# Optimization experiments

Measured on AMD Instinct MI355X. Metric: run time of the kernel, lower is better.

## Reference

```python
import jax, jax.numpy as jnp
import numpy as np
from jax.ops import segment_sum, segment_max

N_NODES, N_EDGES, N_GRAPHS = 50000, 800000, 128
IN_C, HID, HEADS, CLIN = 64, 64, 4, 32


def gat_layer(x, W, a_s, a_d, b, src, dst, n):
    # GAT-style attention conv with concatenated heads (PyG GATConv math).
    H, C = a_s.shape
    h = (x @ W).reshape(-1, H, C)                      # [N,H,C]
    es = jnp.einsum('nhc,hc->nh', h, a_s)
    ed = jnp.einsum('nhc,hc->nh', h, a_d)
    e = jax.nn.leaky_relu(es[src] + ed[dst], 0.2)      # [E,H]
    m = segment_max(e, dst, num_segments=n)            # stable softmax over incoming edges
    e = jnp.exp(e - m[dst])
    denom = segment_sum(e, dst, num_segments=n)
    alpha = e / jnp.where(denom[dst] > 0, denom[dst], 1.0)
    out = segment_sum(h[src] * alpha[:, :, None], dst, num_segments=n)  # [N,H,C]
    return out.reshape(-1, H * C) + b


def label_prop(x, src, dst, n, num_layers=2, alpha=0.5):
    # PyG LabelPropagation: sym-normalized diffusion, residual mix, clamp to [0,1].
    deg = segment_sum(jnp.ones((src.shape[0],), x.dtype), dst, num_segments=n)
    dis = jnp.where(deg > 0, 1.0 / jnp.sqrt(jnp.maximum(deg, 1.0)), 0.0)
    norm = (dis[src] * dis[dst])[:, None]
    res = (1.0 - alpha) * x
    out = x
    for _ in range(num_layers):
        out = alpha * segment_sum(out[src] * norm, dst, num_segments=n) + res
        out = jnp.clip(out, 0.0, 1.0)
    return out


def mean_pool(x, batch, n_graphs):
    cnt = segment_sum(jnp.ones((x.shape[0],), x.dtype), batch, num_segments=n_graphs)
    s = segment_sum(x, batch, num_segments=n_graphs)
    return s / jnp.maximum(cnt, 1.0)[:, None]


def setup_inputs() -> dict:
    key = jax.random.key(0)
    ks = iter(jax.random.split(key, 32))
    def p(shape, fan_in):
        return jax.random.normal(next(ks), shape, jnp.float32) / np.sqrt(fan_in)
    d = {}
    d['x'] = jax.random.normal(next(ks), (N_NODES, IN_C), jnp.float32)
    d['edge_index'] = jax.random.randint(next(ks), (2, N_EDGES), 0, N_NODES)
    d['batch'] = jnp.sort(jax.random.randint(next(ks), (N_NODES,), 0, N_GRAPHS))
    d['clinical_data'] = jax.random.normal(next(ks), (N_GRAPHS, CLIN), jnp.float32)
    HC = HEADS * HID
    d['W1'] = p((IN_C, HC), IN_C); d['a1s'] = p((HEADS, HID), HID); d['a1d'] = p((HEADS, HID), HID); d['b1'] = jnp.zeros((HC,), jnp.float32)
    d['W2'] = p((HC, HC), HC); d['a2s'] = p((HEADS, HID), HID); d['a2d'] = p((HEADS, HID), HID); d['b2'] = jnp.zeros((HC,), jnp.float32)
    jk = IN_C + 2 * HC  # 576
    d['pp_w1'] = p((jk, 256), jk); d['pp_b1'] = jnp.zeros((256,), jnp.float32)
    d['pp_w2'] = p((256, 128), 256); d['pp_b2'] = jnp.zeros((128,), jnp.float32)
    d['cl_w1'] = p((CLIN, 64), CLIN); d['cl_b1'] = jnp.zeros((64,), jnp.float32)
    d['cl_w2'] = p((64, 32), 64); d['cl_b2'] = jnp.zeros((32,), jnp.float32)
    d['h_w1'] = p((160, 64), 160); d['h_b1'] = jnp.zeros((64,), jnp.float32)
    d['h_w2'] = p((64, 32), 64); d['h_b2'] = jnp.zeros((32,), jnp.float32)
    d['h_w3'] = p((32, 2), 32); d['h_b3'] = jnp.zeros((2,), jnp.float32)
    return d


def reference(x, edge_index, batch, clinical_data,
              W1, a1s, a1d, b1, W2, a2s, a2d, b2,
              pp_w1, pp_b1, pp_w2, pp_b2,
              cl_w1, cl_b1, cl_w2, cl_b2,
              h_w1, h_b1, h_w2, h_b2, h_w3, h_b3):
    src, dst = edge_index[0], edge_index[1]
    n = x.shape[0]
    h0 = x
    h1 = jax.nn.relu(gat_layer(h0, W1, a1s, a1d, b1, src, dst, n))
    h1 = label_prop(h1, src, dst, n)
    h2 = jax.nn.relu(gat_layer(h1, W2, a2s, a2d, b2, src, dst, n))
    h2 = label_prop(h2, src, dst, n)
    combined = jnp.concatenate([h0, h1, h2], axis=-1)           # [N, 576]
    g = mean_pool(combined, batch, N_GRAPHS)                    # [G, 576]
    v_graph = jax.nn.relu(g @ pp_w1 + pp_b1) @ pp_w2 + pp_b2    # [G, 128] (dropout = eval/no-op)
    v_clin = jax.nn.relu(clinical_data @ cl_w1 + cl_b1) @ cl_w2 + cl_b2  # [G, 32]
    z = jnp.concatenate([v_graph, v_clin], axis=-1)             # [G, 160]
    z = jax.nn.relu(z @ h_w1 + h_b1)
    z = jax.nn.relu(z @ h_w2 + h_b2)
    return z @ h_w3 + h_b3                                      # [G, 2]
```

## Files before the change

kernel.cpp:

```cpp
#include <hip/hip_runtime.h>

#define N_NODES 50000
#define N_EDGES 800000
#define N_GRAPHS 128
#define JK 576
#define CAP 192
#define NSB ((N_NODES + 255) / 256)

typedef __attribute__((ext_vector_type(8))) short bf16x8;
typedef __attribute__((ext_vector_type(4))) float f32x4;

__device__ __forceinline__ unsigned f2_to_bf2(float a, float b) {
    unsigned ua = __float_as_uint(a), ub = __float_as_uint(b);
    ua = (ua + 0x7fffu + ((ua >> 16) & 1u)) >> 16;
    ub = (ub + 0x7fffu + ((ub >> 16) & 1u)) >> 16;
    return ua | (ub << 16);
}
__device__ __forceinline__ uint2 f4_to_bf4(float4 v) {
    return make_uint2(f2_to_bf2(v.x, v.y), f2_to_bf2(v.z, v.w));
}
__device__ __forceinline__ float4 bf4_to_f4(uint2 u) {
    float4 r;
    r.x = __uint_as_float(u.x << 16);
    r.y = __uint_as_float(u.x & 0xffff0000u);
    r.z = __uint_as_float(u.y << 16);
    r.w = __uint_as_float(u.y & 0xffff0000u);
    return r;
}

template<int BN, int KK>
__global__ __launch_bounds__(256)
void mfma_gemm(const unsigned short* __restrict__ Abf, int lda,
               const unsigned short* __restrict__ BT,
               unsigned* __restrict__ Cbf, int ldc,
               int M, const float* __restrict__ bias, int relu,
               int a_off, int b_off, int c_off) {
    __shared__ unsigned short As[64][32];
    __shared__ unsigned short Bs[BN][32];
    const int t = threadIdx.x;
    const int wav = t >> 6, lane = t & 63;
    const int quad = lane >> 4, l15 = lane & 15;
    const int m0 = blockIdx.x * 64;
    const int head = blockIdx.y;
    Abf += (size_t)head * a_off;
    BT  += (size_t)head * b_off;
    const float* bptr = bias ? bias + (size_t)head * c_off : nullptr;
    unsigned* cbf = Cbf + (((size_t)head * c_off) >> 1);

    f32x4 acc[BN / 16];
#pragma unroll
    for (int i = 0; i < BN / 16; i++) acc[i] = (f32x4){0.f, 0.f, 0.f, 0.f};

    const int arow = t >> 2, aseg = t & 3;
    for (int k0 = 0; k0 < KK; k0 += 32) {
        uint4 av = make_uint4(0, 0, 0, 0);
        int gm = m0 + arow;
        if (gm < M) av = *(const uint4*)&Abf[(size_t)gm * lda + k0 + aseg * 8];
        uint4 bv[BN == 256 ? 4 : 1];
        if (BN == 256) {
            const unsigned short* srcb = &BT[(size_t)t * KK + k0];
#pragma unroll
            for (int j = 0; j < 4; j++) bv[j] = *(const uint4*)&srcb[j * 8];
        } else {
            bv[0] = *(const uint4*)&BT[(size_t)arow * KK + k0 + aseg * 8];
        }
        __syncthreads();
        *(uint4*)&As[arow][aseg * 8] = av;
        if (BN == 256) {
#pragma unroll
            for (int j = 0; j < 4; j++) *(uint4*)&Bs[t][j * 8] = bv[j];
        } else {
            *(uint4*)&Bs[arow][aseg * 8] = bv[0];
        }
        __syncthreads();
        bf16x8 afrag = *(const bf16x8*)&As[wav * 16 + l15][quad * 8];
#pragma unroll
        for (int nt = 0; nt < BN / 16; nt++) {
            bf16x8 bfrag = *(const bf16x8*)&Bs[nt * 16 + l15][quad * 8];
            acc[nt] = __builtin_amdgcn_mfma_f32_16x16x32_bf16(afrag, bfrag, acc[nt], 0, 0, 0);
        }
    }
    int rbase = m0 + wav * 16 + quad * 4;
#pragma unroll
    for (int nt = 0; nt < BN / 16; nt++) {
        int col = nt * 16 + l15;
        float bb = bptr ? bptr[col] : 0.f;
#pragma unroll
        for (int r = 0; r < 4; r++) {
            int row = rbase + r;
            float v = acc[nt][r] + bb;
            if (relu) v = fmaxf(v, 0.f);
            float vp = __shfl_xor(v, 1);
            if (row < M && !(l15 & 1))
                cbf[((size_t)row * ldc + col) >> 1] = f2_to_bf2(v, vp);
        }
    }
}

__global__ void conv_wT(const float* __restrict__ W, unsigned short* __restrict__ WT,
                        int IN, int OUT) {
    int i = blockIdx.x * blockDim.x + threadIdx.x;
    if (i >= IN * OUT) return;
    int n = i / IN, c = i - n * IN;
    unsigned u = __float_as_uint(W[(size_t)c * OUT + n]);
    u = (u + 0x7fffu + ((u >> 16) & 1u)) >> 16;
    WT[i] = (unsigned short)u;
}

__global__ void deg_kernel(const int* __restrict__ dst, int* __restrict__ deg) {
    int t = blockIdx.x * blockDim.x + threadIdx.x;
    if (t < N_EDGES) atomicAdd(&deg[dst[t]], 1);
}
__global__ void dis_kernel(const int* __restrict__ deg, float* __restrict__ dis) {
    int i = blockIdx.x * blockDim.x + threadIdx.x;
    if (i >= N_NODES) return;
    int d = deg[i];
    dis[i] = d > 0 ? rsqrtf((float)d) : 0.f;
}
__global__ __launch_bounds__(256) void scan_bsum(const int* __restrict__ deg,
                                                 int* __restrict__ bsum) {
    __shared__ int sd[256];
    int n = blockIdx.x * 256 + threadIdx.x;
    sd[threadIdx.x] = (n < N_NODES) ? deg[n] : 0;
    __syncthreads();
    for (int o = 128; o > 0; o >>= 1) {
        if (threadIdx.x < o) sd[threadIdx.x] += sd[threadIdx.x + o];
        __syncthreads();
    }
    if (threadIdx.x == 0) bsum[blockIdx.x] = sd[0];
}
__global__ __launch_bounds__(256) void scan_bpre(const int* __restrict__ bsum,
                                                 int* __restrict__ bpre,
                                                 int* __restrict__ off_last) {
    __shared__ int sd[256];
    int t = threadIdx.x;
    int v = (t < NSB) ? bsum[t] : 0;
    sd[t] = v;
    __syncthreads();
    for (int o = 1; o < 256; o <<= 1) {
        int u = (t >= o) ? sd[t - o] : 0;
        __syncthreads();
        sd[t] += u;
        __syncthreads();
    }
    if (t < NSB) bpre[t] = sd[t] - v;
    if (t == 255) *off_last = sd[255];
}
__global__ __launch_bounds__(256) void scan_off(const int* __restrict__ deg,
                                                const int* __restrict__ bpre,
                                                int* __restrict__ off) {
    __shared__ int sd[256];
    int n = blockIdx.x * 256 + threadIdx.x;
    int t = threadIdx.x;
    int v = (n < N_NODES) ? deg[n] : 0;
    sd[t] = v;
    __syncthreads();
    for (int o = 1; o < 256; o <<= 1) {
        int u = (t >= o) ? sd[t - o] : 0;
        __syncthreads();
        sd[t] += u;
        __syncthreads();
    }
    if (n < N_NODES) off[n] = bpre[blockIdx.x] + sd[t] - v;
}
__global__ void csr_fill(const int* __restrict__ src, const int* __restrict__ dst,
                         const int* __restrict__ off, int* __restrict__ cursor,
                         int* __restrict__ csr_src) {
    int e = blockIdx.x * blockDim.x + threadIdx.x;
    if (e >= N_EDGES) return;
    int s = src[e], d = dst[e];
    int pos = off[d] + atomicAdd(&cursor[d], 1);
    csr_src[pos] = s;
}

__global__ void prep_w(const float* __restrict__ W, const float* __restrict__ as_,
                       const float* __restrict__ ad_, float* __restrict__ wes,
                       float* __restrict__ wed, int K) {
    int t = blockIdx.x * blockDim.x + threadIdx.x;
    if (t >= K * 4) return;
    int c = t >> 2, h = t & 3;
    float se = 0.f, sd = 0.f;
    for (int j = 0; j < 64; j++) {
        float w = W[(size_t)c * 256 + h * 64 + j];
        se += w * as_[h * 64 + j];
        sd += w * ad_[h * 64 + j];
    }
    wes[c * 4 + h] = se;
    wed[c * 4 + h] = sd;
}

__global__ void esed_x(const float* __restrict__ X, const float* __restrict__ wes,
                       const float* __restrict__ wed, float* __restrict__ es,
                       float* __restrict__ ed) {
    int gid = blockIdx.x * blockDim.x + threadIdx.x;
    int n = gid >> 6, lane = threadIdx.x & 63;
    if (n >= N_NODES) return;
    float xv = X[(size_t)n * 64 + lane];
    float4 a = *(const float4*)&wes[lane * 4];
    float4 b = *(const float4*)&wed[lane * 4];
    float4 ps = make_float4(xv * a.x, xv * a.y, xv * a.z, xv * a.w);
    float4 pd = make_float4(xv * b.x, xv * b.y, xv * b.z, xv * b.w);
#pragma unroll
    for (int o = 1; o < 64; o <<= 1) {
        ps.x += __shfl_xor(ps.x, o); ps.y += __shfl_xor(ps.y, o);
        ps.z += __shfl_xor(ps.z, o); ps.w += __shfl_xor(ps.w, o);
        pd.x += __shfl_xor(pd.x, o); pd.y += __shfl_xor(pd.y, o);
        pd.z += __shfl_xor(pd.z, o); pd.w += __shfl_xor(pd.w, o);
    }
    if (lane == 0) {
        *(float4*)&es[n * 4] = ps;
        *(float4*)&ed[n * 4] = pd;
    }
}

__global__ void esed_h(const unsigned* __restrict__ Hbf, const float* __restrict__ wes,
                       const float* __restrict__ wed, float* __restrict__ es,
                       float* __restrict__ ed) {
    int gid = blockIdx.x * blockDim.x + threadIdx.x;
    int n = gid >> 6, lane = threadIdx.x & 63;
    if (n >= N_NODES) return;
    float4 xv = bf4_to_f4(*(const uint2*)&Hbf[(size_t)n * 128 + lane * 2]);
    float xs[4] = {xv.x, xv.y, xv.z, xv.w};
    float4 ps = make_float4(0.f, 0.f, 0.f, 0.f);
    float4 pd = make_float4(0.f, 0.f, 0.f, 0.f);
#pragma unroll
    for (int r = 0; r < 4; r++) {
        int c = lane * 4 + r;
        float4 a = *(const float4*)&wes[c * 4];
        float4 b = *(const float4*)&wed[c * 4];
        ps.x += xs[r] * a.x; ps.y += xs[r] * a.y; ps.z += xs[r] * a.z; ps.w += xs[r] * a.w;
        pd.x += xs[r] * b.x; pd.y += xs[r] * b.y; pd.z += xs[r] * b.z; pd.w += xs[r] * b.w;
    }
#pragma unroll
    for (int o = 1; o < 64; o <<= 1) {
        ps.x += __shfl_xor(ps.x, o); ps.y += __shfl_xor(ps.y, o);
        ps.z += __shfl_xor(ps.z, o); ps.w += __shfl_xor(ps.w, o);
        pd.x += __shfl_xor(pd.x, o); pd.y += __shfl_xor(pd.y, o);
        pd.z += __shfl_xor(pd.z, o); pd.w += __shfl_xor(pd.w, o);
    }
    if (lane == 0) {
        *(float4*)&es[n * 4] = ps;
        *(float4*)&ed[n * 4] = pd;
    }
}

__global__ __launch_bounds__(256)
void gat1_fused(const int* __restrict__ off, const int* __restrict__ csr_src,
                const float* __restrict__ es, const float* __restrict__ ed,
                const float* __restrict__ x, unsigned* __restrict__ aggx_bf,
                float* __restrict__ alpha_fb) {
    __shared__ float elds[4][CAP * 4];
    __shared__ int   sidx[4][CAP];
    int wav = threadIdx.x >> 6, lane = threadIdx.x & 63;
    int n = blockIdx.x * 4 + wav;
    bool active = n < N_NODES;
    int p0 = 0, p1 = 0;
    float4 ed4 = make_float4(0.f, 0.f, 0.f, 0.f);
    if (active) { p0 = off[n]; p1 = off[n + 1]; ed4 = *(const float4*)&ed[n * 4]; }
    float4 sum = make_float4(0.f, 0.f, 0.f, 0.f);
    for (int p = p0 + lane; p < p1; p += 64) {
        int s = csr_src[p];
        float4 e4 = *(const float4*)&es[s * 4];
        e4.x += ed4.x; e4.y += ed4.y; e4.z += ed4.z; e4.w += ed4.w;
        e4.x = e4.x > 0.f ? e4.x : 0.2f * e4.x;
        e4.y = e4.y > 0.f ? e4.y : 0.2f * e4.y;
        e4.z = e4.z > 0.f ? e4.z : 0.2f * e4.z;
        e4.w = e4.w > 0.f ? e4.w : 0.2f * e4.w;
        e4.x = __expf(e4.x); e4.y = __expf(e4.y); e4.z = __expf(e4.z); e4.w = __expf(e4.w);
        int q = p - p0;
        if (q < CAP) { *(float4*)&elds[wav][q * 4] = e4; sidx[wav][q] = s; }
        else         *(float4*)&alpha_fb[(size_t)p * 4] = e4;
        sum.x += e4.x; sum.y += e4.y; sum.z += e4.z; sum.w += e4.w;
    }
#pragma unroll
    for (int o = 1; o < 64; o <<= 1) {
        sum.x += __shfl_xor(sum.x, o); sum.y += __shfl_xor(sum.y, o);
        sum.z += __shfl_xor(sum.z, o); sum.w += __shfl_xor(sum.w, o);
    }
    float4 rs;
    rs.x = sum.x > 0.f ? 1.f / sum.x : 0.f;
    rs.y = sum.y > 0.f ? 1.f / sum.y : 0.f;
    rs.z = sum.z > 0.f ? 1.f / sum.z : 0.f;
    rs.w = sum.w > 0.f ? 1.f / sum.w : 0.f;
    if (!active) return;
    int eg = lane >> 4, l15 = lane & 15;
    int deg = p1 - p0;
    float4 a0 = make_float4(0.f, 0.f, 0.f, 0.f);
    float4 a1 = a0, a2 = a0, a3 = a0;
    int q = eg;
    float4 eA = make_float4(0.f, 0.f, 0.f, 0.f);
    float4 xA = eA;
    if (q < deg) {
        int s;
        if (q < CAP) { s = sidx[wav][q]; eA = *(const float4*)&elds[wav][q * 4]; }
        else { s = csr_src[p0 + q]; eA = *(const float4*)&alpha_fb[(size_t)(p0 + q) * 4]; }
        xA = *(const float4*)&x[(size_t)s * 64 + l15 * 4];
    }
    while (q < deg) {
        int qn = q + 4;
        float4 eB = make_float4(0.f, 0.f, 0.f, 0.f);
        float4 xB = eB;
        if (qn < deg) {
            int s;
            if (qn < CAP) { s = sidx[wav][qn]; eB = *(const float4*)&elds[wav][qn * 4]; }
            else { s = csr_src[p0 + qn]; eB = *(const float4*)&alpha_fb[(size_t)(p0 + qn) * 4]; }
            xB = *(const float4*)&x[(size_t)s * 64 + l15 * 4];
        }
        a0.x += eA.x * xA.x; a0.y += eA.x * xA.y; a0.z += eA.x * xA.z; a0.w += eA.x * xA.w;
        a1.x += eA.y * xA.x; a1.y += eA.y * xA.y; a1.z += eA.y * xA.z; a1.w += eA.y * xA.w;
        a2.x += eA.z * xA.x; a2.y += eA.z * xA.y; a2.z += eA.z * xA.z; a2.w += eA.z * xA.w;
        a3.x += eA.w * xA.x; a3.y += eA.w * xA.y; a3.z += eA.w * xA.z; a3.w += eA.w * xA.w;
        eA = eB; xA = xB; q = qn;
    }
#pragma unroll
    for (int o = 16; o < 64; o <<= 1) {
        a0.x += __shfl_xor(a0.x, o); a0.y += __shfl_xor(a0.y, o);
        a0.z += __shfl_xor(a0.z, o); a0.w += __shfl_xor(a0.w, o);
        a1.x += __shfl_xor(a1.x, o); a1.y += __shfl_xor(a1.y, o);
        a1.z += __shfl_xor(a1.z, o); a1.w += __shfl_xor(a1.w, o);
        a2.x += __shfl_xor(a2.x, o); a2.y += __shfl_xor(a2.y, o);
        a2.z += __shfl_xor(a2.z, o); a2.w += __shfl_xor(a2.w, o);
        a3.x += __shfl_xor(a3.x, o); a3.y += __shfl_xor(a3.y, o);
        a3.z += __shfl_xor(a3.z, o); a3.w += __shfl_xor(a3.w, o);
    }
    if (eg == 0) {
        a0.x *= rs.x; a0.y *= rs.x; a0.z *= rs.x; a0.w *= rs.x;
        a1.x *= rs.y; a1.y *= rs.y; a1.z *= rs.y; a1.w *= rs.y;
        a2.x *= rs.z; a2.y *= rs.z; a2.z *= rs.z; a2.w *= rs.z;
        a3.x *= rs.w; a3.y *= rs.w; a3.z *= rs.w; a3.w *= rs.w;
        size_t b = (size_t)n * 128 + l15 * 2;
        *(uint2*)&aggx_bf[b +  0] = f4_to_bf4(a0);
        *(uint2*)&aggx_bf[b + 32] = f4_to_bf4(a1);
        *(uint2*)&aggx_bf[b + 64] = f4_to_bf4(a2);
        *(uint2*)&aggx_bf[b + 96] = f4_to_bf4(a3);
    }
}

__global__ __launch_bounds__(256)
void gat2_fused(const int* __restrict__ off, const int* __restrict__ csr_src,
                const float* __restrict__ es, const float* __restrict__ ed,
                const unsigned* __restrict__ H2bf, const float* __restrict__ bias,
                unsigned* __restrict__ outbf, float* __restrict__ alpha_fb) {
    __shared__ float elds[4][CAP * 4];
    __shared__ int   sidx[4][CAP];
    int wav = threadIdx.x >> 6, lane = threadIdx.x & 63;
    int n = blockIdx.x * 4 + wav;
    bool active = n < N_NODES;
    int p0 = 0, p1 = 0;
    float4 ed4 = make_float4(0.f, 0.f, 0.f, 0.f);
    if (active) { p0 = off[n]; p1 = off[n + 1]; ed4 = *(const float4*)&ed[n * 4]; }
    float4 sum = make_float4(0.f, 0.f, 0.f, 0.f);
    for (int p = p0 + lane; p < p1; p += 64) {
        int s = csr_src[p];
        float4 e4 = *(const float4*)&es[s * 4];
        e4.x += ed4.x; e4.y += ed4.y; e4.z += ed4.z; e4.w += ed4.w;
        e4.x = e4.x > 0.f ? e4.x : 0.2f * e4.x;
        e4.y = e4.y > 0.f ? e4.y : 0.2f * e4.y;
        e4.z = e4.z > 0.f ? e4.z : 0.2f * e4.z;
        e4.w = e4.w > 0.f ? e4.w : 0.2f * e4.w;
        e4.x = __expf(e4.x); e4.y = __expf(e4.y); e4.z = __expf(e4.z); e4.w = __expf(e4.w);
        int q = p - p0;
        if (q < CAP) { *(float4*)&elds[wav][q * 4] = e4; sidx[wav][q] = s; }
        else         *(float4*)&alpha_fb[(size_t)p * 4] = e4;
        sum.x += e4.x; sum.y += e4.y; sum.z += e4.z; sum.w += e4.w;
    }
#pragma unroll
    for (int o = 1; o < 64; o <<= 1) {
        sum.x += __shfl_xor(sum.x, o); sum.y += __shfl_xor(sum.y, o);
        sum.z += __shfl_xor(sum.z, o); sum.w += __shfl_xor(sum.w, o);
    }
    if (!active) return;
    int half = lane >> 5, l = lane & 31;
    int hh = l >> 3;
    float sh = (hh == 0) ? sum.x : (hh == 1) ? sum.y : (hh == 2) ? sum.z : sum.w;
    float rsh = sh > 0.f ? 1.f / sh : 0.f;
    int deg = p1 - p0;
    float acc[8];
#pragma unroll
    for (int j = 0; j < 8; j++) acc[j] = 0.f;
    int q = half;
    float aA = 0.f;
    uint4 rA = make_uint4(0, 0, 0, 0);
    if (q < deg) {
        int s;
        if (q < CAP) { s = sidx[wav][q]; aA = elds[wav][q * 4 + hh]; }
        else { s = csr_src[p0 + q]; aA = alpha_fb[(size_t)(p0 + q) * 4 + hh]; }
        rA = *(const uint4*)&H2bf[(size_t)s * 128 + l * 4];
    }
    while (q < deg) {
        int qn = q + 2;
        float aB = 0.f;
        uint4 rB = make_uint4(0, 0, 0, 0);
        if (qn < deg) {
            int s;
            if (qn < CAP) { s = sidx[wav][qn]; aB = elds[wav][qn * 4 + hh]; }
            else { s = csr_src[p0 + qn]; aB = alpha_fb[(size_t)(p0 + qn) * 4 + hh]; }
            rB = *(const uint4*)&H2bf[(size_t)s * 128 + l * 4];
        }
        float4 f0 = bf4_to_f4(make_uint2(rA.x, rA.y));
        float4 f1 = bf4_to_f4(make_uint2(rA.z, rA.w));
        acc[0] += aA * f0.x; acc[1] += aA * f0.y; acc[2] += aA * f0.z; acc[3] += aA * f0.w;
        acc[4] += aA * f1.x; acc[5] += aA * f1.y; acc[6] += aA * f1.z; acc[7] += aA * f1.w;
        aA = aB; rA = rB; q = qn;
    }
#pragma unroll
    for (int j = 0; j < 8; j++) acc[j] += __shfl_xor(acc[j], 32);
    if (half == 0) {
        float4 b0 = *(const float4*)&bias[l * 8];
        float4 b1 = *(const float4*)&bias[l * 8 + 4];
        float4 o0, o1;
        o0.x = fmaxf(acc[0] * rsh + b0.x, 0.f);
        o0.y = fmaxf(acc[1] * rsh + b0.y, 0.f);
        o0.z = fmaxf(acc[2] * rsh + b0.z, 0.f);
        o0.w = fmaxf(acc[3] * rsh + b0.w, 0.f);
        o1.x = fmaxf(acc[4] * rsh + b1.x, 0.f);
        o1.y = fmaxf(acc[5] * rsh + b1.y, 0.f);
        o1.z = fmaxf(acc[6] * rsh + b1.z, 0.f);
        o1.w = fmaxf(acc[7] * rsh + b1.w, 0.f);
        uint2 w0 = f4_to_bf4(o0), w1 = f4_to_bf4(o1);
        uint4 w = make_uint4(w0.x, w0.y, w1.x, w1.y);
        *(uint4*)&outbf[(size_t)n * 128 + l * 4] = w;
    }
}

__global__ __launch_bounds__(256)
void lp_csr(const int* __restrict__ off, const int* __restrict__ csr_src,
            const float* __restrict__ dis, const unsigned* __restrict__ in_bf,
            const unsigned* __restrict__ res_bf, unsigned* __restrict__ out_bf) {
    __shared__ int   widx[4][CAP];
    __shared__ float wwt[4][CAP];
    int wav = threadIdx.x >> 6, lane = threadIdx.x & 63;
    int n = blockIdx.x * 4 + wav;
    if (n >= N_NODES) return;
    int p0 = off[n], p1 = off[n + 1];
    int deg = p1 - p0;
    float disd = dis[n];
    for (int q = lane; q < deg && q < CAP; q += 64) {
        int s = csr_src[p0 + q];
        widx[wav][q] = s;
        wwt[wav][q] = dis[s] * disd;
    }
    int half = lane >> 5, l = lane & 31;
    float acc[8];
#pragma unroll
    for (int j = 0; j < 8; j++) acc[j] = 0.f;
    int q = half;
    float nA = 0.f;
    uint4 rA = make_uint4(0, 0, 0, 0);
    if (q < deg) {
        int s;
        if (q < CAP) { s = widx[wav][q]; nA = wwt[wav][q]; }
        else { s = csr_src[p0 + q]; nA = dis[s] * disd; }
        rA = *(const uint4*)&in_bf[(size_t)s * 128 + l * 4];
    }
    while (q < deg) {
        int qn = q + 2;
        float nB = 0.f;
        uint4 rB = make_uint4(0, 0, 0, 0);
        if (qn < deg) {
            int s;
            if (qn < CAP) { s = widx[wav][qn]; nB = wwt[wav][qn]; }
            else { s = csr_src[p0 + qn]; nB = dis[s] * disd; }
            rB = *(const uint4*)&in_bf[(size_t)s * 128 + l * 4];
        }
        float4 f0 = bf4_to_f4(make_uint2(rA.x, rA.y));
        float4 f1 = bf4_to_f4(make_uint2(rA.z, rA.w));
        acc[0] += nA * f0.x; acc[1] += nA * f0.y; acc[2] += nA * f0.z; acc[3] += nA * f0.w;
        acc[4] += nA * f1.x; acc[5] += nA * f1.y; acc[6] += nA * f1.z; acc[7] += nA * f1.w;
        nA = nB; rA = rB; q = qn;
    }
#pragma unroll
    for (int j = 0; j < 8; j++) acc[j] += __shfl_xor(acc[j], 32);
    if (half == 0) {
        uint4 rr = *(const uint4*)&res_bf[(size_t)n * 128 + l * 4];
        float4 r0 = bf4_to_f4(make_uint2(rr.x, rr.y));
        float4 r1 = bf4_to_f4(make_uint2(rr.z, rr.w));
        float4 o0, o1;
        o0.x = fminf(fmaxf(0.5f * acc[0] + 0.5f * r0.x, 0.f), 1.f);
        o0.y = fminf(fmaxf(0.5f * acc[1] + 0.5f * r0.y, 0.f), 1.f);
        o0.z = fminf(fmaxf(0.5f * acc[2] + 0.5f * r0.z, 0.f), 1.f);
        o0.w = fminf(fmaxf(0.5f * acc[3] + 0.5f * r0.w, 0.f), 1.f);
        o1.x = fminf(fmaxf(0.5f * acc[4] + 0.5f * r1.x, 0.f), 1.f);
        o1.y = fminf(fmaxf(0.5f * acc[5] + 0.5f * r1.y, 0.f), 1.f);
        o1.z = fminf(fmaxf(0.5f * acc[6] + 0.5f * r1.z, 0.f), 1.f);
        o1.w = fminf(fmaxf(0.5f * acc[7] + 0.5f * r1.w, 0.f), 1.f);
        uint2 w0 = f4_to_bf4(o0), w1 = f4_to_bf4(o1);
        uint4 w = make_uint4(w0.x, w0.y, w1.x, w1.y);
        *(uint4*)&out_bf[(size_t)n * 128 + l * 4] = w;
    }
}

__global__ void bounds_kernel(const int* __restrict__ batch, int* __restrict__ gstart) {
    int n = blockIdx.x * blockDim.x + threadIdx.x;
    if (n >= N_NODES) return;
    int b = batch[n];
    int prev = (n == 0) ? -1 : batch[n - 1];
    for (int g = prev + 1; g <= b; g++) gstart[g] = n;
    if (n == N_NODES - 1)
        for (int g = b + 1; g <= N_GRAPHS; g++) gstart[g] = N_NODES;
}
__global__ void pool_partial(const float* __restrict__ buf, const int* __restrict__ gstart,
                             float* __restrict__ psum, int C, int colOff) {
    int g = blockIdx.x, q = blockIdx.y;
    int n0 = gstart[g], n1 = gstart[g + 1];
    int len = n1 - n0;
    int ns = n0 + (len * q) / 4, ne = n0 + (len * (q + 1)) / 4;
    int cp = threadIdx.x % C;
    int np = threadIdx.x / C;
    int NP = 256 / C;
    float s = 0.f;
    for (int n = ns + np; n < ne; n += NP) s += buf[(size_t)n * C + cp];
    atomicAdd(&psum[g * JK + colOff + cp], s);
}
__global__ void pool_bf(const unsigned* __restrict__ buf, const int* __restrict__ gstart,
                        float* __restrict__ psum, int colOff) {
    int g = blockIdx.x, q = blockIdx.y;
    int n0 = gstart[g], n1 = gstart[g + 1];
    int len = n1 - n0;
    int ns = n0 + (len * q) / 4, ne = n0 + (len * (q + 1)) / 4;
    int cp = threadIdx.x & 127;
    int np = threadIdx.x >> 7;
    float s0 = 0.f, s1 = 0.f;
    for (int n = ns + np; n < ne; n += 2) {
        unsigned u = buf[(size_t)n * 128 + cp];
        s0 += __uint_as_float(u << 16);
        s1 += __uint_as_float(u & 0xffff0000u);
    }
    atomicAdd(&psum[g * JK + colOff + cp * 2 + 0], s0);
    atomicAdd(&psum[g * JK + colOff + cp * 2 + 1], s1);
}
__global__ void gmean_kernel(const float* __restrict__ psum, const int* __restrict__ gstart,
                             float* __restrict__ g) {
    int i = blockIdx.x * blockDim.x + threadIdx.x;
    if (i >= N_GRAPHS * JK) return;
    int gi = i / JK;
    int len = gstart[gi + 1] - gstart[gi];
    g[i] = psum[i] / (float)(len > 1 ? len : 1);
}

__global__ __launch_bounds__(64)
void head_d1(const float* __restrict__ gbuf, const float* __restrict__ W,
             const float* __restrict__ bias, float* __restrict__ out) {
    __shared__ float zin[JK];
    int g = blockIdx.y, mc = blockIdx.x, lane = threadIdx.x;
    for (int k = lane; k < JK; k += 64) zin[k] = gbuf[g * JK + k];
    __syncthreads();
    int m = mc * 64 + lane;
    float acc = bias[m];
#pragma unroll 8
    for (int k = 0; k < JK; k++) acc += zin[k] * W[k * 256 + m];
    out[g * 256 + m] = fmaxf(acc, 0.f);
}

__global__ __launch_bounds__(256)
void head_rest(const float* __restrict__ t1, const float* __restrict__ clin,
               const float* __restrict__ pp_w2, const float* __restrict__ pp_b2,
               const float* __restrict__ cl_w1, const float* __restrict__ cl_b1,
               const float* __restrict__ cl_w2, const float* __restrict__ cl_b2,
               const float* __restrict__ h_w1, const float* __restrict__ h_b1,
               const float* __restrict__ h_w2, const float* __restrict__ h_b2,
               const float* __restrict__ h_w3, const float* __restrict__ h_b3,
               float* __restrict__ out) {
    __shared__ float z1[256];
    __shared__ float zcl[32];
    __shared__ float zc[64];
    __shared__ float z[160];
    __shared__ float z3[64];
    __shared__ float z4[32];
    __shared__ float part[128];
    int g = blockIdx.x, t = threadIdx.x;
    z1[t] = t1[g * 256 + t];
    if (t < 32) zcl[t] = clin[g * 32 + t];
    __syncthreads();
    int m = t & 127, half = t >> 7;
    {
        float acc = 0.f;
        int k0 = half * 128;
#pragma unroll 8
        for (int k = k0; k < k0 + 128; k++) acc += z1[k] * pp_w2[k * 128 + m];
        if (half) part[m] = acc;
        __syncthreads();
        if (!half) z[m] = acc + part[m] + pp_b2[m];
    }
    if (t < 64) {
        float acc = cl_b1[t];
#pragma unroll
        for (int k = 0; k < 32; k++) acc += zcl[k] * cl_w1[k * 64 + t];
        zc[t] = fmaxf(acc, 0.f);
    }
    __syncthreads();
    if (t < 32) {
        float acc = cl_b2[t];
#pragma unroll
        for (int k = 0; k < 64; k++) acc += zc[k] * cl_w2[k * 32 + t];
        z[128 + t] = acc;
    }
    __syncthreads();
    if (t < 64) {
        float acc = h_b1[t];
#pragma unroll 8
        for (int k = 0; k < 160; k++) acc += z[k] * h_w1[k * 64 + t];
        z3[t] = fmaxf(acc, 0.f);
    }
    __syncthreads();
    if (t < 32) {
        float acc = h_b2[t];
#pragma unroll
        for (int k = 0; k < 64; k++) acc += z3[k] * h_w2[k * 32 + t];
        z4[t] = fmaxf(acc, 0.f);
    }
    __syncthreads();
    if (t < 2) {
        float acc = h_b3[t];
#pragma unroll
        for (int k = 0; k < 32; k++) acc += z4[k] * h_w3[k * 2 + t];
        out[g * 2 + t] = acc;
    }
}

extern "C" void kernel_launch(void* const* d_in, const int* in_sizes, int n_in,
                              void* d_out, int out_size, void* d_ws, size_t ws_size,
                              hipStream_t stream) {
    const float* x     = (const float*)d_in[0];
    const int*   ei    = (const int*)d_in[1];
    const int*   batch = (const int*)d_in[2];
    const float* clin  = (const float*)d_in[3];
    const float* W1  = (const float*)d_in[4];
    const float* a1s = (const float*)d_in[5];
    const float* a1d = (const float*)d_in[6];
    const float* b1  = (const float*)d_in[7];
    const float* W2  = (const float*)d_in[8];
    const float* a2s = (const float*)d_in[9];
    const float* a2d = (const float*)d_in[10];
    const float* b2  = (const float*)d_in[11];
    const float* pp_w1 = (const float*)d_in[12];
    const float* pp_b1 = (const float*)d_in[13];
    const float* pp_w2 = (const float*)d_in[14];
    const float* pp_b2 = (const float*)d_in[15];
    const float* cl_w1 = (const float*)d_in[16];
    const float* cl_b1 = (const float*)d_in[17];
    const float* cl_w2 = (const float*)d_in[18];
    const float* cl_b2 = (const float*)d_in[19];
    const float* h_w1  = (const float*)d_in[20];
    const float* h_b1  = (const float*)d_in[21];
    const float* h_w2  = (const float*)d_in[22];
    const float* h_b2  = (const float*)d_in[23];
    const float* h_w3  = (const float*)d_in[24];
    const float* h_b3  = (const float*)d_in[25];

    const int* src = ei;
    const int* dst = ei + N_EDGES;

    char* p = (char*)d_ws;
    auto carve = [&](size_t bytes) -> char* {
        char* r = p;
        p += (bytes + 255) & ~(size_t)255;
        return r;
    };
    const size_t NBH = (size_t)N_NODES * 256 * 2;
    unsigned* abf  = (unsigned*)carve(NBH);
    unsigned* bf1  = (unsigned*)carve(NBH);
    unsigned* bf2  = (unsigned*)carve(NBH);
    unsigned* bf3  = (unsigned*)carve(NBH);
    float* alpha_fb  = (float*)carve((size_t)N_EDGES * 4 * 4);
    int*   csr_src   = (int*)carve((size_t)N_EDGES * 4);
    int*   off       = (int*)carve((size_t)(N_NODES + 1) * 4);
    int*   deg       = (int*)carve((size_t)N_NODES * 4);
    int*   cursor    = (int*)carve((size_t)N_NODES * 4);
    int*   bsum      = (int*)carve((size_t)NSB * 4);
    int*   bpre      = (int*)carve((size_t)NSB * 4);
    float* dis       = (float*)carve((size_t)N_NODES * 4);
    float* es        = (float*)carve((size_t)N_NODES * 4 * 4);
    float* ed        = (float*)carve((size_t)N_NODES * 4 * 4);
    float* wes1      = (float*)carve((size_t)64 * 4 * 4);
    float* wed1      = (float*)carve((size_t)64 * 4 * 4);
    float* wes2      = (float*)carve((size_t)256 * 4 * 4);
    float* wed2      = (float*)carve((size_t)256 * 4 * 4);
    unsigned short* W1T = (unsigned short*)carve((size_t)256 * 64 * 2);
    unsigned short* W2T = (unsigned short*)carve((size_t)256 * 256 * 2);
    int*   gstart    = (int*)carve((size_t)(N_GRAPHS + 1) * 4);
    float* psum      = (float*)carve((size_t)N_GRAPHS * JK * 4);
    float* gbuf      = (float*)carve((size_t)N_GRAPHS * JK * 4);
    float* t1        = (float*)carve((size_t)N_GRAPHS * 256 * 4);

    const int TB = 256;
    const int gN     = (N_NODES + TB - 1) / TB;
    const int gE     = (N_EDGES + TB - 1) / TB;
    const int gNwave = (N_NODES * 64 + TB - 1) / TB;
    const int gFuse  = (N_NODES + 3) / 4;
    const int gRow   = (N_NODES + 63) / 64;

    hipMemsetAsync(deg, 0, (size_t)N_NODES * 4, stream);
    hipMemsetAsync(cursor, 0, (size_t)N_NODES * 4, stream);
    hipMemsetAsync(psum, 0, (size_t)N_GRAPHS * JK * 4, stream);
    deg_kernel<<<gE, TB, 0, stream>>>(dst, deg);
    dis_kernel<<<gN, TB, 0, stream>>>(deg, dis);
    scan_bsum<<<NSB, 256, 0, stream>>>(deg, bsum);
    scan_bpre<<<1, 256, 0, stream>>>(bsum, bpre, &off[N_NODES]);
    scan_off<<<NSB, 256, 0, stream>>>(deg, bpre, off);
    csr_fill<<<gE, TB, 0, stream>>>(src, dst, off, cursor, csr_src);
    bounds_kernel<<<gN, TB, 0, stream>>>(batch, gstart);
    prep_w<<<1, 256, 0, stream>>>(W1, a1s, a1d, wes1, wed1, 64);
    prep_w<<<4, 256, 0, stream>>>(W2, a2s, a2d, wes2, wed2, 256);
    conv_wT<<<(256 * 64 + TB - 1) / TB, TB, 0, stream>>>(W1, W1T, 64, 256);
    conv_wT<<<(256 * 256 + TB - 1) / TB, TB, 0, stream>>>(W2, W2T, 256, 256);

    esed_x<<<gNwave, TB, 0, stream>>>(x, wes1, wed1, es, ed);
    gat1_fused<<<gFuse, TB, 0, stream>>>(off, csr_src, es, ed, x, abf, alpha_fb);
    mfma_gemm<64, 64><<<dim3(gRow, 4), 256, 0, stream>>>(
        (const unsigned short*)abf, 256, W1T, bf1, 256, N_NODES, b1, 1,
        64, 64 * 64, 64);

    lp_csr<<<gFuse, TB, 0, stream>>>(off, csr_src, dis, bf1, bf1, bf2);
    lp_csr<<<gFuse, TB, 0, stream>>>(off, csr_src, dis, bf2, bf1, bf3);

    pool_bf<<<dim3(N_GRAPHS, 4), TB, 0, stream>>>(bf3, gstart, psum, 64);

    mfma_gemm<256, 256><<<dim3(gRow, 1), 256, 0, stream>>>(
        (const unsigned short*)bf3, 256, W2T, bf1, 256, N_NODES, nullptr, 0,
        0, 0, 0);
    esed_h<<<gNwave, TB, 0, stream>>>(bf3, wes2, wed2, es, ed);
    gat2_fused<<<gFuse, TB, 0, stream>>>(off, csr_src, es, ed, bf1, b2, bf2, alpha_fb);

    lp_csr<<<gFuse, TB, 0, stream>>>(off, csr_src, dis, bf2, bf2, bf1);
    lp_csr<<<gFuse, TB, 0, stream>>>(off, csr_src, dis, bf1, bf2, abf);

    pool_partial<<<dim3(N_GRAPHS, 4), TB, 0, stream>>>(x, gstart, psum, 64, 0);
    pool_bf<<<dim3(N_GRAPHS, 4), TB, 0, stream>>>(abf, gstart, psum, 320);
    gmean_kernel<<<(N_GRAPHS * JK + TB - 1) / TB, TB, 0, stream>>>(psum, gstart, gbuf);

    head_d1<<<dim3(4, N_GRAPHS), 64, 0, stream>>>(gbuf, pp_w1, pp_b1, t1);
    head_rest<<<N_GRAPHS, 256, 0, stream>>>(t1, clin, pp_w2, pp_b2, cl_w1, cl_b1,
                                            cl_w2, cl_b2, h_w1, h_b1, h_w2, h_b2,
                                            h_w3, h_b3, (float*)d_out);
}
```

Baseline: 798.3 us.

## Merge prep kernels, gather bf16 features in GAT1, deepen gather prefetch

Folds the small setup kernels (dis, graph bounds, attention weight projection, weight transposes) into one launch. The same launch also converts x to bf16 so GAT layer 1 gathers half as many bytes per neighbour. The gather loops in gat1, gat2 and label propagation now keep three edges of loads in flight instead of one, to hide memory latency. The cost is more registers per thread, and rounding x to bf16 before aggregation adds some precision loss.

```diff
diff --git a/kernel.cpp b/kernel.cpp
--- a/kernel.cpp
+++ b/kernel.cpp
@@ -97,25 +97,78 @@
     }
 }
 
-__global__ void conv_wT(const float* __restrict__ W, unsigned short* __restrict__ WT,
-                        int IN, int OUT) {
-    int i = blockIdx.x * blockDim.x + threadIdx.x;
-    if (i >= IN * OUT) return;
-    int n = i / IN, c = i - n * IN;
-    unsigned u = __float_as_uint(W[(size_t)c * OUT + n]);
-    u = (u + 0x7fffu + ((u >> 16) & 1u)) >> 16;
-    WT[i] = (unsigned short)u;
-}
-
 __global__ void deg_kernel(const int* __restrict__ dst, int* __restrict__ deg) {
     int t = blockIdx.x * blockDim.x + threadIdx.x;
     if (t < N_EDGES) atomicAdd(&deg[dst[t]], 1);
 }
-__global__ void dis_kernel(const int* __restrict__ deg, float* __restrict__ dis) {
+#define S1 50000
+#define S2 100000
+#define S3 100256
+#define S4 101280
+#define S5 117664
+#define S6 183200
+#define S7 1783200
+__global__ void prep_misc(const int* __restrict__ deg, float* __restrict__ dis,
+                          const int* __restrict__ batch, int* __restrict__ gstart,
+                          const float* __restrict__ W1, const float* __restrict__ a1s,
+                          const float* __restrict__ a1d, float* __restrict__ wes1,
+                          float* __restrict__ wed1,
+                          const float* __restrict__ W2, const float* __restrict__ a2s,
+                          const float* __restrict__ a2d, float* __restrict__ wes2,
+                          float* __restrict__ wed2,
+                          unsigned short* __restrict__ W1T, unsigned short* __restrict__ W2T,
+                          const float* __restrict__ x, unsigned* __restrict__ xbf) {
     int i = blockIdx.x * blockDim.x + threadIdx.x;
-    if (i >= N_NODES) return;
-    int d = deg[i];
-    dis[i] = d > 0 ? rsqrtf((float)d) : 0.f;
+    if (i >= S7) return;
+    if (i >= S6) {
+        int j = i - S6;
+        float2 v = *(const float2*)&x[(size_t)j * 2];
+        xbf[j] = f2_to_bf2(v.x, v.y);
+    } else if (i >= S5) {
+        int t2 = i - S5;
+        int n = t2 >> 8, c = t2 & 255;
+        unsigned u = __float_as_uint(W2[(size_t)c * 256 + n]);
+        u = (u + 0x7fffu + ((u >> 16) & 1u)) >> 16;
+        W2T[t2] = (unsigned short)u;
+    } else if (i >= S4) {
+        int t2 = i - S4;
+        int n = t2 >> 6, c = t2 & 63;
+        unsigned u = __float_as_uint(W1[(size_t)c * 256 + n]);
+        u = (u + 0x7fffu + ((u >> 16) & 1u)) >> 16;
+        W1T[t2] = (unsigned short)u;
+    } else if (i >= S3) {
+        int t2 = i - S3;
+        int c = t2 >> 2, h = t2 & 3;
+        float se = 0.f, sd = 0.f;
+        for (int j = 0; j < 64; j++) {
+            float w = W2[(size_t)c * 256 + h * 64 + j];
+            se += w * a2s[h * 64 + j];
+            sd += w * a2d[h * 64 + j];
+        }
+        wes2[c * 4 + h] = se;
+        wed2[c * 4 + h] = sd;
+    } else if (i >= S2) {
+        int t2 = i - S2;
+        int c = t2 >> 2, h = t2 & 3;
+        float se = 0.f, sd = 0.f;
+        for (int j = 0; j < 64; j++) {
+            float w = W1[(size_t)c * 256 + h * 64 + j];
+            se += w * a1s[h * 64 + j];
+            sd += w * a1d[h * 64 + j];
+        }
+        wes1[c * 4 + h] = se;
+        wed1[c * 4 + h] = sd;
+    } else if (i >= S1) {
+        int n = i - S1;
+        int b = batch[n];
+        int prev = (n == 0) ? -1 : batch[n - 1];
+        for (int g = prev + 1; g <= b; g++) gstart[g] = n;
+        if (n == N_NODES - 1)
+            for (int g = b + 1; g <= N_GRAPHS; g++) gstart[g] = N_NODES;
+    } else {
+        int d = deg[i];
+        dis[i] = d > 0 ? rsqrtf((float)d) : 0.f;
+    }
 }
 __global__ __launch_bounds__(256) void scan_bsum(const int* __restrict__ deg,
                                                  int* __restrict__ bsum) {
@@ -171,22 +224,6 @@
     int s = src[e], d = dst[e];
     int pos = off[d] + atomicAdd(&cursor[d], 1);
     csr_src[pos] = s;
-}
-
-__global__ void prep_w(const float* __restrict__ W, const float* __restrict__ as_,
-                       const float* __restrict__ ad_, float* __restrict__ wes,
-                       float* __restrict__ wed, int K) {
-    int t = blockIdx.x * blockDim.x + threadIdx.x;
-    if (t >= K * 4) return;
-    int c = t >> 2, h = t & 3;
-    float se = 0.f, sd = 0.f;
-    for (int j = 0; j < 64; j++) {
-        float w = W[(size_t)c * 256 + h * 64 + j];
-        se += w * as_[h * 64 + j];
-        sd += w * ad_[h * 64 + j];
-    }
-    wes[c * 4 + h] = se;
-    wed[c * 4 + h] = sd;
 }
 
 __global__ void esed_x(const float* __restrict__ X, const float* __restrict__ wes,
@@ -247,7 +284,7 @@
 __global__ __launch_bounds__(256)
 void gat1_fused(const int* __restrict__ off, const int* __restrict__ csr_src,
                 const float* __restrict__ es, const float* __restrict__ ed,
-                const float* __restrict__ x, unsigned* __restrict__ aggx_bf,
+                const unsigned* __restrict__ xbf, unsigned* __restrict__ aggx_bf,
                 float* __restrict__ alpha_fb) {
     __shared__ float elds[4][CAP * 4];
     __shared__ int   sidx[4][CAP];
@@ -287,30 +324,30 @@
     int deg = p1 - p0;
     float4 a0 = make_float4(0.f, 0.f, 0.f, 0.f);
     float4 a1 = a0, a2 = a0, a3 = a0;
+    auto fetch = [&](int qq, float4& e4, float4& xv) {
+        e4 = make_float4(0.f, 0.f, 0.f, 0.f);
+        xv = e4;
+        if (qq < deg) {
+            int s;
+            if (qq < CAP) { s = sidx[wav][qq]; e4 = *(const float4*)&elds[wav][qq * 4]; }
+            else { s = csr_src[p0 + qq]; e4 = *(const float4*)&alpha_fb[(size_t)(p0 + qq) * 4]; }
+            xv = bf4_to_f4(*(const uint2*)&xbf[(size_t)s * 32 + l15 * 2]);
+        }
+    };
     int q = eg;
-    float4 eA = make_float4(0.f, 0.f, 0.f, 0.f);
-    float4 xA = eA;
-    if (q < deg) {
-        int s;
-        if (q < CAP) { s = sidx[wav][q]; eA = *(const float4*)&elds[wav][q * 4]; }
-        else { s = csr_src[p0 + q]; eA = *(const float4*)&alpha_fb[(size_t)(p0 + q) * 4]; }
-        xA = *(const float4*)&x[(size_t)s * 64 + l15 * 4];
-    }
+    float4 eA, xA, eB, xB, eC, xC;
+    fetch(q, eA, xA);
+    fetch(q + 4, eB, xB);
+    fetch(q + 8, eC, xC);
     while (q < deg) {
-        int qn = q + 4;
-        float4 eB = make_float4(0.f, 0.f, 0.f, 0.f);
-        float4 xB = eB;
-        if (qn < deg) {
-            int s;
-            if (qn < CAP) { s = sidx[wav][qn]; eB = *(const float4*)&elds[wav][qn * 4]; }
-            else { s = csr_src[p0 + qn]; eB = *(const float4*)&alpha_fb[(size_t)(p0 + qn) * 4]; }
-            xB = *(const float4*)&x[(size_t)s * 64 + l15 * 4];
-        }
+        float4 eD, xD;
+        fetch(q + 12, eD, xD);
         a0.x += eA.x * xA.x; a0.y += eA.x * xA.y; a0.z += eA.x * xA.z; a0.w += eA.x * xA.w;
         a1.x += eA.y * xA.x; a1.y += eA.y * xA.y; a1.z += eA.y * xA.z; a1.w += eA.y * xA.w;
         a2.x += eA.z * xA.x; a2.y += eA.z * xA.y; a2.z += eA.z * xA.z; a2.w += eA.z * xA.w;
         a3.x += eA.w * xA.x; a3.y += eA.w * xA.y; a3.z += eA.w * xA.z; a3.w += eA.w * xA.w;
-        eA = eB; xA = xB; q = qn;
+        eA = eB; xA = xB; eB = eC; xB = xC; eC = eD; xC = xD;
+        q += 4;
     }
 #pragma unroll
     for (int o = 16; o < 64; o <<= 1) {
@@ -378,30 +415,31 @@
     float acc[8];
 #pragma unroll
     for (int j = 0; j < 8; j++) acc[j] = 0.f;
+    auto fetch = [&](int qq, float& al, uint4& rr) {
+        al = 0.f;
+        rr = make_uint4(0, 0, 0, 0);
+        if (qq < deg) {
+            int s;
+            if (qq < CAP) { s = sidx[wav][qq]; al = elds[wav][qq * 4 + hh]; }
+            else { s = csr_src[p0 + qq]; al = alpha_fb[(size_t)(p0 + qq) * 4 + hh]; }
+            rr = *(const uint4*)&H2bf[(size_t)s * 128 + l * 4];
+        }
+    };
     int q = half;
-    float aA = 0.f;
-    uint4 rA = make_uint4(0, 0, 0, 0);
-    if (q < deg) {
-        int s;
-        if (q < CAP) { s = sidx[wav][q]; aA = elds[wav][q * 4 + hh]; }
-        else { s = csr_src[p0 + q]; aA = alpha_fb[(size_t)(p0 + q) * 4 + hh]; }
-        rA = *(const uint4*)&H2bf[(size_t)s * 128 + l * 4];
-    }
+    float aA, aB, aC;
+    uint4 rA, rB, rC;
+    fetch(q, aA, rA);
+    fetch(q + 2, aB, rB);
+    fetch(q + 4, aC, rC);
     while (q < deg) {
-        int qn = q + 2;
-        float aB = 0.f;
-        uint4 rB = make_uint4(0, 0, 0, 0);
-        if (qn < deg) {
-            int s;
-            if (qn < CAP) { s = sidx[wav][qn]; aB = elds[wav][qn * 4 + hh]; }
-            else { s = csr_src[p0 + qn]; aB = alpha_fb[(size_t)(p0 + qn) * 4 + hh]; }
-            rB = *(const uint4*)&H2bf[(size_t)s * 128 + l * 4];
-        }
+        float aD; uint4 rD;
+        fetch(q + 6, aD, rD);
         float4 f0 = bf4_to_f4(make_uint2(rA.x, rA.y));
         float4 f1 = bf4_to_f4(make_uint2(rA.z, rA.w));
         acc[0] += aA * f0.x; acc[1] += aA * f0.y; acc[2] += aA * f0.z; acc[3] += aA * f0.w;
         acc[4] += aA * f1.x; acc[5] += aA * f1.y; acc[6] += aA * f1.z; acc[7] += aA * f1.w;
-        aA = aB; rA = rB; q = qn;
+        aA = aB; rA = rB; aB = aC; rB = rC; aC = aD; rC = rD;
+        q += 2;
     }
 #pragma unroll
     for (int j = 0; j < 8; j++) acc[j] += __shfl_xor(acc[j], 32);
@@ -444,30 +482,31 @@
     float acc[8];
 #pragma unroll
     for (int j = 0; j < 8; j++) acc[j] = 0.f;
+    auto fetch = [&](int qq, float& nw, uint4& rr) {
+        nw = 0.f;
+        rr = make_uint4(0, 0, 0, 0);
+        if (qq < deg) {
+            int s;
+            if (qq < CAP) { s = widx[wav][qq]; nw = wwt[wav][qq]; }
+            else { s = csr_src[p0 + qq]; nw = dis[s] * disd; }
+            rr = *(const uint4*)&in_bf[(size_t)s * 128 + l * 4];
+        }
+    };
     int q = half;
-    float nA = 0.f;
-    uint4 rA = make_uint4(0, 0, 0, 0);
-    if (q < deg) {
-        int s;
-        if (q < CAP) { s = widx[wav][q]; nA = wwt[wav][q]; }
-        else { s = csr_src[p0 + q]; nA = dis[s] * disd; }
-        rA = *(const uint4*)&in_bf[(size_t)s * 128 + l * 4];
-    }
+    float nA, nB, nC;
+    uint4 rA, rB, rC;
+    fetch(q, nA, rA);
+    fetch(q + 2, nB, rB);
+    fetch(q + 4, nC, rC);
     while (q < deg) {
-        int qn = q + 2;
-        float nB = 0.f;
-        uint4 rB = make_uint4(0, 0, 0, 0);
-        if (qn < deg) {
-            int s;
-            if (qn < CAP) { s = widx[wav][qn]; nB = wwt[wav][qn]; }
-            else { s = csr_src[p0 + qn]; nB = dis[s] * disd; }
-            rB = *(const uint4*)&in_bf[(size_t)s * 128 + l * 4];
-        }
+        float nD; uint4 rD;
+        fetch(q + 6, nD, rD);
         float4 f0 = bf4_to_f4(make_uint2(rA.x, rA.y));
         float4 f1 = bf4_to_f4(make_uint2(rA.z, rA.w));
         acc[0] += nA * f0.x; acc[1] += nA * f0.y; acc[2] += nA * f0.z; acc[3] += nA * f0.w;
         acc[4] += nA * f1.x; acc[5] += nA * f1.y; acc[6] += nA * f1.z; acc[7] += nA * f1.w;
-        nA = nB; rA = rB; q = qn;
+        nA = nB; rA = rB; nB = nC; rB = rC; nC = nD; rC = rD;
+        q += 2;
     }
 #pragma unroll
     for (int j = 0; j < 8; j++) acc[j] += __shfl_xor(acc[j], 32);
@@ -490,15 +529,6 @@
     }
 }
 
-__global__ void bounds_kernel(const int* __restrict__ batch, int* __restrict__ gstart) {
-    int n = blockIdx.x * blockDim.x + threadIdx.x;
-    if (n >= N_NODES) return;
-    int b = batch[n];
-    int prev = (n == 0) ? -1 : batch[n - 1];
-    for (int g = prev + 1; g <= b; g++) gstart[g] = n;
-    if (n == N_NODES - 1)
-        for (int g = b + 1; g <= N_GRAPHS; g++) gstart[g] = N_NODES;
-}
 __global__ void pool_partial(const float* __restrict__ buf, const int* __restrict__ gstart,
                              float* __restrict__ psum, int C, int colOff) {
     int g = blockIdx.x, q = blockIdx.y;
@@ -662,6 +692,7 @@
     unsigned* bf1  = (unsigned*)carve(NBH);
     unsigned* bf2  = (unsigned*)carve(NBH);
     unsigned* bf3  = (unsigned*)carve(NBH);
+    unsigned* xbf  = (unsigned*)carve((size_t)N_NODES * 32 * 4);
     float* alpha_fb  = (float*)carve((size_t)N_EDGES * 4 * 4);
     int*   csr_src   = (int*)carve((size_t)N_EDGES * 4);
     int*   off       = (int*)carve((size_t)(N_NODES + 1) * 4);
@@ -684,29 +715,27 @@
     float* t1        = (float*)carve((size_t)N_GRAPHS * 256 * 4);
 
     const int TB = 256;
-    const int gN     = (N_NODES + TB - 1) / TB;
     const int gE     = (N_EDGES + TB - 1) / TB;
     const int gNwave = (N_NODES * 64 + TB - 1) / TB;
     const int gFuse  = (N_NODES + 3) / 4;
     const int gRow   = (N_NODES + 63) / 64;
+    const int gPrep  = (S7 + TB - 1) / TB;
 
     hipMemsetAsync(deg, 0, (size_t)N_NODES * 4, stream);
     hipMemsetAsync(cursor, 0, (size_t)N_NODES * 4, stream);
     hipMemsetAsync(psum, 0, (size_t)N_GRAPHS * JK * 4, stream);
     deg_kernel<<<gE, TB, 0, stream>>>(dst, deg);
-    dis_kernel<<<gN, TB, 0, stream>>>(deg, dis);
+    prep_misc<<<gPrep, TB, 0, stream>>>(deg, dis, batch, gstart,
+                                        W1, a1s, a1d, wes1, wed1,
+                                        W2, a2s, a2d, wes2, wed2,
+                                        W1T, W2T, x, xbf);
     scan_bsum<<<NSB, 256, 0, stream>>>(deg, bsum);
     scan_bpre<<<1, 256, 0, stream>>>(bsum, bpre, &off[N_NODES]);
     scan_off<<<NSB, 256, 0, stream>>>(deg, bpre, off);
     csr_fill<<<gE, TB, 0, stream>>>(src, dst, off, cursor, csr_src);
-    bounds_kernel<<<gN, TB, 0, stream>>>(batch, gstart);
-    prep_w<<<1, 256, 0, stream>>>(W1, a1s, a1d, wes1, wed1, 64);
-    prep_w<<<4, 256, 0, stream>>>(W2, a2s, a2d, wes2, wed2, 256);
-    conv_wT<<<(256 * 64 + TB - 1) / TB, TB, 0, stream>>>(W1, W1T, 64, 256);
-    conv_wT<<<(256 * 256 + TB - 1) / TB, TB, 0, stream>>>(W2, W2T, 256, 256);
 
     esed_x<<<gNwave, TB, 0, stream>>>(x, wes1, wed1, es, ed);
-    gat1_fused<<<gFuse, TB, 0, stream>>>(off, csr_src, es, ed, x, abf, alpha_fb);
+    gat1_fused<<<gFuse, TB, 0, stream>>>(off, csr_src, es, ed, xbf, abf, alpha_fb);
     mfma_gemm<64, 64><<<dim3(gRow, 4), 256, 0, stream>>>(
         (const unsigned short*)abf, 256, W1T, bf1, 256, N_NODES, b1, 1,
         64, 64 * 64, 64);
```

Result: no change. 784.3 us (-1.8%).
